# Optimization experiments

Measured on AMD Instinct MI355X. Metric: run time of the kernel, lower is better.

The kernel has to match this reference:

```python
import math
import jax, jax.numpy as jnp
import numpy as np

SIZE = 5
MUL = 16                      # multiplicity of 0e and 1o in irreps_in and irreps_out
DIM = 4 * MUL                 # 16x0e (16) + 16x1o (48) = 64
INV_SQRT3 = 1.0 / math.sqrt(3.0)          # nonzero entries of wigner_3j for (1,1,0),(0,1,1),(1,0,1)
ALPHA_0 = math.sqrt(1.0 / (2 * MUL))      # out 0e: ir.dim=1 / (two uvw paths, 16*1 elements each)
ALPHA_1 = math.sqrt(3.0 / (2 * MUL))      # out 1o: ir.dim=3 / (two uvw paths, 16*1 elements each)


def _lattice():
    # torch.linspace(-1,1,size), meshgrid 'ij'; steps=(1,1,1) keeps the full cube
    r = np.linspace(-1.0, 1.0, SIZE, dtype=np.float32)
    gx, gy, gz = np.meshgrid(r, r, r, indexing='ij')
    lat = np.stack([gx, gy, gz], axis=-1)                      # (S,S,S,3), order (x,y,z)
    d = np.linalg.norm(lat, axis=-1)
    unit = np.where(d[..., None] > 0, lat / np.maximum(d[..., None], 1e-12), 0.0)
    # e3nn spherical harmonics, normalize=True, 'component' norm; l=1 basis order (y,z,x)
    sh0 = np.ones_like(d)                                      # l=0 component-normalized
    sh1 = math.sqrt(3.0) * unit[..., [1, 2, 0]]                # (S,S,S,3)
    return jnp.asarray(d), jnp.asarray(sh0), jnp.asarray(sh1)


def soft_one_hot_linspace(x, start, end, number):
    sigma = (end - start) / (number - 1)
    values = jnp.linspace(start, end, number, dtype=x.dtype)
    return jnp.exp(-(((x[..., None] - values) / sigma) ** 2)) / 1.12


def setup_inputs() -> dict:
    key = jax.random.key(0)
    k1, k2, k3, k4 = jax.random.split(key, 4)
    return {
        'x': jax.random.normal(k1, (2, DIM, 64, 64, 64), dtype=jnp.float32),
        'lin_w0': jax.random.normal(k2, (MUL, MUL), dtype=jnp.float32),
        'lin_w1': jax.random.normal(k3, (MUL, MUL), dtype=jnp.float32),
        'tp_weight': jax.random.normal(k4, (SIZE, 4 * MUL * MUL), dtype=jnp.float32),
    }


def reference(x, lin_w0, lin_w1, tp_weight):
    d, sh0, sh1 = _lattice()
    B, _, X, Y, Z = x.shape

    # ---- self connection: e3nn Linear per irrep, scaled by 1/sqrt(fan_in) ----
    inv = 1.0 / math.sqrt(MUL)
    x0 = x[:, :MUL]                                            # (B,16,X,Y,Z) scalars
    x1 = x[:, MUL:].reshape(B, MUL, 3, X, Y, Z)                # (B,16,3,X,Y,Z) vectors
    sc0 = jnp.einsum('uw,buxyz->bwxyz', lin_w0, x0) * inv
    sc1 = jnp.einsum('uw,buixyz->bwixyz', lin_w1, x1) * inv
    sc = jnp.concatenate([sc0, sc1.reshape(B, 3 * MUL, X, Y, Z)], axis=1)

    # ---- radial weights: soft one-hot embedding @ learned weights ----
    emb = soft_one_hot_linspace(d, 0.0, 1.0, SIZE) @ tp_weight                 # (S,S,S,1024)
    emb = emb * (jnp.cos(math.pi * d) / SIZE ** 1.5)[..., None]
    mm = MUL * MUL
    wA = emb[..., 0 * mm:1 * mm].reshape(SIZE, SIZE, SIZE, MUL, MUL)  # 0e(x)0e->0e
    wB = emb[..., 1 * mm:2 * mm].reshape(SIZE, SIZE, SIZE, MUL, MUL)  # 0e(x)1o->1o
    wC = emb[..., 2 * mm:3 * mm].reshape(SIZE, SIZE, SIZE, MUL, MUL)  # 1o(x)0e->1o
    wD = emb[..., 3 * mm:4 * mm].reshape(SIZE, SIZE, SIZE, MUL, MUL)  # 1o(x)1o->0e

    # ---- tp.right(sh, weight): kernel (S,S,S, in_dim, out_dim) ----
    eye3 = jnp.eye(3, dtype=x.dtype)
    k00 = ALPHA_0 * wA * sh0[..., None, None]                                        # (g,16,16)
    k10 = (ALPHA_0 * INV_SQRT3) * jnp.einsum('...uw,...i->...uiw', wD, sh1)          # (g,16,3,16)
    k01 = (ALPHA_1 * INV_SQRT3) * jnp.einsum('...uw,...k->...uwk', wB, sh1)          # (g,16,16,3)
    k11 = (ALPHA_1 * INV_SQRT3) * jnp.einsum('...uw,ik->...uiwk',
                                             wC * sh0[..., None, None], eye3)        # (g,16,3,16,3)
    g = (SIZE, SIZE, SIZE)
    top = jnp.concatenate([k00, k01.reshape(*g, MUL, 3 * MUL)], axis=-1)             # (g,16,64)
    bot = jnp.concatenate([k10.reshape(*g, 3 * MUL, MUL),
                           k11.reshape(*g, 3 * MUL, 3 * MUL)], axis=-1)              # (g,48,64)
    kernel = jnp.concatenate([top, bot], axis=-2)                                     # (S,S,S,64,64)

    # einsum('xyzio->oixyz') then conv3d (cross-correlation, same as torch)
    kernel_oi = jnp.transpose(kernel, (4, 3, 0, 1, 2))
    p = SIZE // 2
    conv = jax.lax.conv_general_dilated(
        x, kernel_oi, window_strides=(1, 1, 1), padding=[(p, p)] * 3,
        dimension_numbers=('NCDHW', 'OIDHW', 'NCDHW'))
    return sc + 0.1 * conv
```

## Files before the change

### kernel.cpp

```cpp
#include <hip/hip_runtime.h>
#include <hip/hip_bf16.h>
#include <math.h>

typedef __bf16 bf16x8 __attribute__((ext_vector_type(8)));
typedef __bf16 bf16x2 __attribute__((ext_vector_type(2)));
typedef float  f32x4  __attribute__((ext_vector_type(4)));

#define CI_STRIDE 262144
#define B_STRIDE  16777216
#define Z2 68
#define CP 40
#define NROW 12

__global__ __launch_bounds__(256) void gen_w(const float* __restrict__ tp,
                                             const float* __restrict__ lw0,
                                             const float* __restrict__ lw1,
                                             __bf16* __restrict__ Wb) {
    const int t  = blockIdx.x;
    const int dx = t / 25, dy = (t / 5) % 5, dz = t % 5;
    const float rx = -1.f + 0.5f * (float)dx;
    const float ry = -1.f + 0.5f * (float)dy;
    const float rz = -1.f + 0.5f * (float)dz;
    const float d    = sqrtf(rx * rx + ry * ry + rz * rz);
    const float invd = (d > 0.f) ? (1.f / d) : 0.f;
    const float SQRT3 = 1.7320508075688772f;
    const float sh1_0 = SQRT3 * ry * invd;
    const float sh1_1 = SQRT3 * rz * invd;
    const float sh1_2 = SQRT3 * rx * invd;
    float basis[5];
#pragma unroll
    for (int m = 0; m < 5; ++m) {
        float u = (d - 0.25f * (float)m) * 4.0f;
        basis[m] = expf(-u * u) * (1.0f / 1.12f);
    }
    const float S  = cosf(3.14159265358979323846f * d) * (1.0f / 11.180339887498949f);
    const float fA = 0.1f * 0.17677669529663687f * S;
    const float fB = 0.1f * 0.3061862178478972f * 0.5773502691896258f * S;
    const float fC = 0.1f * 0.17677669529663687f * 0.5773502691896258f * S;
    const float fD = fB;

    for (int e = threadIdx.x; e < 4096; e += 256) {
        const int co = e >> 6, ci = e & 63;
        int   tt;
        float f;
        if (ci < 16) {
            if (co < 16) { tt = ci * 16 + co; f = fA; }
            else {
                const int c = co - 16, w = c / 3, kk = c % 3;
                tt = 256 + ci * 16 + w;
                f  = fB * ((kk == 0) ? sh1_0 : (kk == 1) ? sh1_1 : sh1_2);
            }
        } else {
            const int a = ci - 16, uu = a / 3, ii = a % 3;
            const float s1i = (ii == 0) ? sh1_0 : (ii == 1) ? sh1_1 : sh1_2;
            if (co < 16) { tt = 768 + uu * 16 + co; f = fC * s1i; }
            else {
                const int c = co - 16, w = c / 3, kk = c % 3;
                tt = 512 + uu * 16 + w;
                f  = (ii == kk) ? fD : 0.0f;
            }
        }
        float E = 0.f;
#pragma unroll
        for (int m = 0; m < 5; ++m) E += basis[m] * tp[m * 1024 + tt];
        float val = f * E;
        if (t == 62) {
            if (ci < 16 && co < 16) {
                val += 0.25f * lw0[ci * 16 + co];
            } else if (ci >= 16 && co >= 16) {
                const int a = co - 16, bq = ci - 16;
                const int wq = a / 3, iq = a % 3, uq = bq / 3, iiq = bq % 3;
                if (iq == iiq) val += 0.25f * lw1[uq * 16 + wq];
            }
        }
        Wb[((size_t)(t * 2 + (ci >> 5)) * 64 + co) * 32 + (ci & 31)] = (__bf16)val;
    }
}

__global__ __launch_bounds__(256, 2) void conv_mfma(const float* __restrict__ x,
                                                    const __bf16* __restrict__ Wb,
                                                    float* __restrict__ out) {
    __shared__ __align__(16) __bf16 xs[NROW * Z2 * CP];
    const int tid = threadIdx.x;
    const int l = tid & 63, w = tid >> 6;
    const int q = l >> 4, i16 = l & 15;
    const int b  = blockIdx.x >> 9;
    const int xc = (blockIdx.x >> 3) & 63;
    const int y0 = (blockIdx.x & 7) << 3;

    f32x4 acc[4][8];
#pragma unroll
    for (int mt = 0; mt < 4; ++mt)
#pragma unroll
        for (int nt = 0; nt < 8; ++nt) acc[mt][nt] = (f32x4)(0.f);

    if (tid < NROW * 4 * 4) {
        const int r = tid >> 4, rem = tid & 15;
        const int zs = rem >> 2, c8 = (rem & 3) << 3;
        const int zp = (zs < 2) ? zs : (64 + zs);
        bf16x8 zz = {(__bf16)0.f, (__bf16)0.f, (__bf16)0.f, (__bf16)0.f,
                     (__bf16)0.f, (__bf16)0.f, (__bf16)0.f, (__bf16)0.f};
        *(bf16x8*)(xs + ((size_t)r * Z2 + zp) * CP + c8) = zz;
    }

    const float* xb = x + (size_t)b * B_STRIDE;

    bf16x8 Acur[4], Anext[4];
#pragma unroll
    for (int mt = 0; mt < 4; ++mt)
        Acur[mt] = *(const bf16x8*)(Wb + ((size_t)(mt * 16 + i16)) * 32 + q * 8);

    for (int h = 0; h < 2; ++h) {
        for (int dx = 0; dx < 5; ++dx) {
            __syncthreads();
            {
                const int xp = xc + dx - 2;
                const bool xok = (xp >= 0) && (xp < 64);
                for (int r = w; r < NROW; r += 4) {
                    const int yp = y0 + r - 2;
                    const bool ok = xok && (yp >= 0) && (yp < 64);
                    const float* src = xb + (size_t)(h * 32) * CI_STRIDE
                                     + (size_t)xp * 4096 + yp * 64 + l;
                    __bf16* dst = xs + ((size_t)r * Z2 + 2 + l) * CP;
                    if (ok) {
#pragma unroll
                        for (int c0 = 0; c0 < 32; c0 += 8) {
                            bf16x8 pk;
#pragma unroll
                            for (int j = 0; j < 8; ++j)
                                pk[j] = (__bf16)src[(size_t)(c0 + j) * CI_STRIDE];
                            *(bf16x8*)(dst + c0) = pk;
                        }
                    } else {
                        bf16x8 zz = {(__bf16)0.f, (__bf16)0.f, (__bf16)0.f, (__bf16)0.f,
                                     (__bf16)0.f, (__bf16)0.f, (__bf16)0.f, (__bf16)0.f};
#pragma unroll
                        for (int c0 = 0; c0 < 32; c0 += 8) *(bf16x8*)(dst + c0) = zz;
                    }
                }
            }
            __syncthreads();

            for (int dydz = 0; dydz < 25; ++dydz) {
                const int t = dx * 25 + dydz;
                const int s = h * 125 + t;
                {
                    const int sn = (s < 249) ? (s + 1) : s;
                    const int hn = sn / 125, tn = sn % 125;
                    const __bf16* wp = Wb + ((size_t)(tn * 2 + hn) * 64 + i16) * 32 + q * 8;
#pragma unroll
                    for (int mt = 0; mt < 4; ++mt)
                        Anext[mt] = *(const bf16x8*)(wp + (size_t)mt * 16 * 32);
                }
                const int dy = dydz / 5, dz = dydz % 5;
                const __bf16* bbase = xs + ((size_t)(2 * w + dy) * Z2 + dz + i16) * CP + q * 8;
                bf16x8 Bf[8];
#pragma unroll
                for (int yy = 0; yy < 2; ++yy)
#pragma unroll
                    for (int zt = 0; zt < 4; ++zt)
                        Bf[yy * 4 + zt] = *(const bf16x8*)(bbase + (size_t)(yy * Z2 + zt * 16) * CP);
                __builtin_amdgcn_s_setprio(1);
#pragma unroll
                for (int mt = 0; mt < 4; ++mt)
#pragma unroll
                    for (int nt = 0; nt < 8; ++nt)
                        acc[mt][nt] = __builtin_amdgcn_mfma_f32_16x16x32_bf16(
                            Acur[mt], Bf[nt], acc[mt][nt], 0, 0, 0);
                __builtin_amdgcn_s_setprio(0);
#pragma unroll
                for (int mt = 0; mt < 4; ++mt) Acur[mt] = Anext[mt];
            }
        }
    }

    const size_t ob = (size_t)b * B_STRIDE + (size_t)xc * 4096;
#pragma unroll
    for (int mt = 0; mt < 4; ++mt)
#pragma unroll
        for (int j = 0; j < 4; ++j) {
            const int co = mt * 16 + q * 4 + j;
            float* op = out + ob + (size_t)co * CI_STRIDE;
#pragma unroll
            for (int nt = 0; nt < 8; ++nt) {
                const int y = y0 + 2 * w + (nt >> 2);
                const int z = (nt & 3) * 16 + i16;
                op[y * 64 + z] = acc[mt][nt][j];
            }
        }
}

extern "C" void kernel_launch(void* const* d_in, const int* in_sizes, int n_in,
                              void* d_out, int out_size, void* d_ws, size_t ws_size,
                              hipStream_t stream) {
    (void)in_sizes; (void)n_in; (void)out_size; (void)ws_size;
    const float* x   = (const float*)d_in[0];
    const float* lw0 = (const float*)d_in[1];
    const float* lw1 = (const float*)d_in[2];
    const float* tp  = (const float*)d_in[3];
    float* out = (float*)d_out;
    __bf16* Wb = (__bf16*)d_ws;

    gen_w<<<125, 256, 0, stream>>>(tp, lw0, lw1, Wb);
    conv_mfma<<<1024, 256, 0, stream>>>(x, Wb, out);
}
```

Before: 567.5 us.

## Switch conv MFMA to 32x32x16 tiles with double-buffered A/B fragment loads

Replaces the 16x16x32 bf16 MFMA tiling with 32x32x16 instructions, so each wave computes 2x4 tiles of 32x32 instead of 4x8 tiles of 16x16. The inner tap loop is restructured into a ping-pong scheme that loads the next tap's LDS B fragments and global weight A fragments while the current tap's MFMAs run. This is meant to cut LDS and register fragment traffic per FLOP and to hide load latency. The trade-offs are higher register pressure from the doubled fragment buffers and a different output write pattern.

```diff
diff --git a/kernel.cpp b/kernel.cpp
--- a/kernel.cpp
+++ b/kernel.cpp
@@ -3,8 +3,7 @@
 #include <math.h>
 
 typedef __bf16 bf16x8 __attribute__((ext_vector_type(8)));
-typedef __bf16 bf16x2 __attribute__((ext_vector_type(2)));
-typedef float  f32x4  __attribute__((ext_vector_type(4)));
+typedef float  f32x16 __attribute__((ext_vector_type(16)));
 
 #define CI_STRIDE 262144
 #define B_STRIDE  16777216
@@ -83,16 +82,15 @@
     __shared__ __align__(16) __bf16 xs[NROW * Z2 * CP];
     const int tid = threadIdx.x;
     const int l = tid & 63, w = tid >> 6;
-    const int q = l >> 4, i16 = l & 15;
     const int b  = blockIdx.x >> 9;
     const int xc = (blockIdx.x >> 3) & 63;
     const int y0 = (blockIdx.x & 7) << 3;
 
-    f32x4 acc[4][8];
-#pragma unroll
-    for (int mt = 0; mt < 4; ++mt)
-#pragma unroll
-        for (int nt = 0; nt < 8; ++nt) acc[mt][nt] = (f32x4)(0.f);
+    f32x16 acc[2][4];
+#pragma unroll
+    for (int am = 0; am < 2; ++am)
+#pragma unroll
+        for (int nt = 0; nt < 4; ++nt) acc[am][nt] = (f32x16)(0.f);
 
     if (tid < NROW * 4 * 4) {
         const int r = tid >> 4, rem = tid & 15;
@@ -105,10 +103,40 @@
 
     const float* xb = x + (size_t)b * B_STRIDE;
 
-    bf16x8 Acur[4], Anext[4];
-#pragma unroll
-    for (int mt = 0; mt < 4; ++mt)
-        Acur[mt] = *(const bf16x8*)(Wb + ((size_t)(mt * 16 + i16)) * 32 + q * 8);
+    const int hi = l >> 5;
+    const int l31 = l & 31;
+    const int lane_lds = (2 * w * Z2 + l31) * CP + hi * 8;
+    const int lane_a   = l31 * 32 + hi * 8;
+
+    auto LOADB = [&](bf16x8* Bf, int tapoff) {
+        const __bf16* bp = xs + lane_lds + tapoff;
+#pragma unroll
+        for (int ks = 0; ks < 2; ++ks)
+#pragma unroll
+            for (int nt = 0; nt < 4; ++nt)
+                Bf[ks * 4 + nt] = *(const bf16x8*)(bp + (nt >> 1) * (Z2 * CP)
+                                                    + (nt & 1) * (32 * CP) + ks * 16);
+    };
+    auto LOADA = [&](bf16x8* Af, const __bf16* wp) {
+        const __bf16* ap = wp + lane_a;
+#pragma unroll
+        for (int am = 0; am < 2; ++am)
+#pragma unroll
+            for (int ks = 0; ks < 2; ++ks)
+                Af[am * 2 + ks] = *(const bf16x8*)(ap + am * 1024 + ks * 16);
+    };
+    auto MSET = [&](const bf16x8* Af, const bf16x8* Bf) {
+        __builtin_amdgcn_s_setprio(1);
+#pragma unroll
+        for (int ks = 0; ks < 2; ++ks)
+#pragma unroll
+            for (int am = 0; am < 2; ++am)
+#pragma unroll
+                for (int nt = 0; nt < 4; ++nt)
+                    acc[am][nt] = __builtin_amdgcn_mfma_f32_32x32x16_bf16(
+                        Af[am * 2 + ks], Bf[ks * 4 + nt], acc[am][nt], 0, 0, 0);
+        __builtin_amdgcn_s_setprio(0);
+    };
 
     for (int h = 0; h < 2; ++h) {
         for (int dx = 0; dx < 5; ++dx) {
@@ -141,51 +169,37 @@
             }
             __syncthreads();
 
-            for (int dydz = 0; dydz < 25; ++dydz) {
-                const int t = dx * 25 + dydz;
-                const int s = h * 125 + t;
-                {
-                    const int sn = (s < 249) ? (s + 1) : s;
-                    const int hn = sn / 125, tn = sn % 125;
-                    const __bf16* wp = Wb + ((size_t)(tn * 2 + hn) * 64 + i16) * 32 + q * 8;
-#pragma unroll
-                    for (int mt = 0; mt < 4; ++mt)
-                        Anext[mt] = *(const bf16x8*)(wp + (size_t)mt * 16 * 32);
-                }
-                const int dy = dydz / 5, dz = dydz % 5;
-                const __bf16* bbase = xs + ((size_t)(2 * w + dy) * Z2 + dz + i16) * CP + q * 8;
-                bf16x8 Bf[8];
-#pragma unroll
-                for (int yy = 0; yy < 2; ++yy)
-#pragma unroll
-                    for (int zt = 0; zt < 4; ++zt)
-                        Bf[yy * 4 + zt] = *(const bf16x8*)(bbase + (size_t)(yy * Z2 + zt * 16) * CP);
-                __builtin_amdgcn_s_setprio(1);
-#pragma unroll
-                for (int mt = 0; mt < 4; ++mt)
-#pragma unroll
-                    for (int nt = 0; nt < 8; ++nt)
-                        acc[mt][nt] = __builtin_amdgcn_mfma_f32_16x16x32_bf16(
-                            Acur[mt], Bf[nt], acc[mt][nt], 0, 0, 0);
-                __builtin_amdgcn_s_setprio(0);
-#pragma unroll
-                for (int mt = 0; mt < 4; ++mt) Acur[mt] = Anext[mt];
-            }
+            const __bf16* wplane = Wb + (size_t)((dx * 25) * 2 + h) * 2048;
+            bf16x8 B0[8], B1[8], A0[4], A1[4];
+            LOADB(B0, 0);
+            LOADA(A0, wplane);
+            int dyn = 0, dzn = 1;
+            for (int i = 0; i < 12; ++i) {
+                LOADB(B1, (dyn * Z2 + dzn) * CP);
+                LOADA(A1, wplane + (size_t)(2 * i + 1) * 4096);
+                if (++dzn == 5) { dzn = 0; ++dyn; }
+                MSET(A0, B0);
+                LOADB(B0, (dyn * Z2 + dzn) * CP);
+                LOADA(A0, wplane + (size_t)(2 * i + 2) * 4096);
+                if (++dzn == 5) { dzn = 0; ++dyn; }
+                MSET(A1, B1);
+            }
+            MSET(A0, B0);
         }
     }
 
     const size_t ob = (size_t)b * B_STRIDE + (size_t)xc * 4096;
 #pragma unroll
-    for (int mt = 0; mt < 4; ++mt)
-#pragma unroll
-        for (int j = 0; j < 4; ++j) {
-            const int co = mt * 16 + q * 4 + j;
-            float* op = out + ob + (size_t)co * CI_STRIDE;
-#pragma unroll
-            for (int nt = 0; nt < 8; ++nt) {
-                const int y = y0 + 2 * w + (nt >> 2);
-                const int z = (nt & 3) * 16 + i16;
-                op[y * 64 + z] = acc[mt][nt][j];
+    for (int am = 0; am < 2; ++am)
+#pragma unroll
+        for (int nt = 0; nt < 4; ++nt) {
+            const int y = y0 + 2 * w + (nt >> 1);
+            const int zb = (nt & 1) * 32 + l31;
+            float* op = out + ob + (size_t)y * 64 + zb;
+#pragma unroll
+            for (int reg = 0; reg < 16; ++reg) {
+                const int co = am * 32 + (reg & 3) + 8 * (reg >> 2) + 4 * hi;
+                op[(size_t)co * CI_STRIDE] = acc[am][nt][reg];
             }
         }
 }
```

New measurement: 609.2 us. 1.07x slower.
